# Performance work log

Measured on AMD Instinct MI355X. Metric: run time of the kernel, lower is better.

Reference implementation:

```python
import jax, jax.numpy as jnp
import numpy as np

NUM_OPS = 8
D = 1024
B = 8192


def setup_inputs() -> dict:
    key = jax.random.key(0)
    k1, k2, k3, k4 = jax.random.split(key, 4)
    x = jax.random.normal(k1, (B, D), dtype=jnp.float32)
    logits = 0.001 * jax.random.normal(k2, (NUM_OPS,), dtype=jnp.float32)
    Ws = jax.random.normal(k3, (NUM_OPS, D, D), dtype=jnp.float32) * (1.0 / np.sqrt(D))
    bs = jax.random.normal(k4, (NUM_OPS, D), dtype=jnp.float32) * 0.01
    return {"x": x, "logits": logits, "Ws": Ws, "bs": bs, "num_on_samples": 2}


def reference(x, logits, Ws, bs, num_on_samples):
    # non_stochastic_call: top-k op selection by architecture logits,
    # dispatch x to the selected ops, sum-combine the results.
    _, top_k_ids = jax.lax.top_k(logits, num_on_samples)  # [k]
    W_sel = jnp.take(Ws, top_k_ids, axis=0)  # [k, D, D]
    b_sel = jnp.take(bs, top_k_ids, axis=0)  # [k, D]
    # each op is Dense(D->D) + relu: [k, B, D]
    op_results = jax.nn.relu(jnp.einsum('bd,kde->kbe', x, W_sel) + b_sel[:, None, :])
    return jnp.sum(op_results, axis=0)  # [B, D]
```

## Files before the change

kernel.cpp:

```cpp
#include <hip/hip_runtime.h>
#include <hip/hip_bf16.h>

#define NUM_OPS 8
#define D 1024
#define B_ROWS 8192

typedef unsigned short ushort_t;
typedef __attribute__((ext_vector_type(8))) short bf16x8;
typedef __attribute__((ext_vector_type(4))) float f32x4;
typedef __attribute__((ext_vector_type(4))) float float4v;
typedef __attribute__((ext_vector_type(8))) unsigned short ushort8;

__device__ __forceinline__ unsigned short f2bf(float f) {
    union { float f; unsigned int u; } v; v.f = f;
    unsigned int u = v.u;
    unsigned int lsb = (u >> 16) & 1u;
    u += 0x7fffu + lsb;
    return (unsigned short)(u >> 16);
}

__device__ __forceinline__ void load_lds16(const void* g, void* l) {
    __builtin_amdgcn_global_load_lds(
        (const __attribute__((address_space(1))) void*)g,
        (__attribute__((address_space(3))) void*)l,
        16, 0, 0);
}

__device__ __forceinline__ void top2(const float* __restrict__ logits, int& i0, int& i1) {
    float best = -__builtin_inff(); i0 = 0;
    for (int i = 0; i < NUM_OPS; ++i) { float v = logits[i]; if (v > best) { best = v; i0 = i; } }
    float best2 = -__builtin_inff(); i1 = 0;
    for (int i = 0; i < NUM_OPS; ++i) {
        if (i == i0) continue;
        float v = logits[i]; if (v > best2) { best2 = v; i1 = i; }
    }
}

__global__ void prep_kernel(const float* __restrict__ x,
                            const float* __restrict__ Ws,
                            const float* __restrict__ logits,
                            ushort_t* __restrict__ xbf,
                            ushort_t* __restrict__ Wt) {
    __shared__ float t[32][33];
    const int bid = blockIdx.x;
    const int tid = threadIdx.x;
    if (bid < 4096) {
        int i = (bid * 256 + tid) * 8;
        float4v v0 = *(const float4v*)(x + i);
        float4v v1 = *(const float4v*)(x + i + 4);
        ushort8 o;
        o[0] = f2bf(v0[0]); o[1] = f2bf(v0[1]); o[2] = f2bf(v0[2]); o[3] = f2bf(v0[3]);
        o[4] = f2bf(v1[0]); o[5] = f2bf(v1[1]); o[6] = f2bf(v1[2]); o[7] = f2bf(v1[3]);
        *(ushort8*)(xbf + i) = o;
    } else {
        int i0, i1; top2(logits, i0, i1);
        const int b  = bid - 4096;
        const int e    = b >> 10;
        const int tile = b & 1023;
        const int td = (tile >> 5) << 5;
        const int te = (tile & 31) << 5;
        const int tx = tid & 31, ty = tid >> 5;
        const float* W = Ws + (size_t)(e ? i1 : i0) * D * D;
        for (int r = 0; r < 4; ++r)
            t[ty + 8 * r][tx] = W[(size_t)(td + ty + 8 * r) * D + te + tx];
        __syncthreads();
        ushort_t* o = Wt + (size_t)e * D * D;
        for (int r = 0; r < 4; ++r)
            o[(size_t)(te + ty + 8 * r) * D + td + tx] = f2bf(t[tx][ty + 8 * r]);
    }
}

__device__ __forceinline__ void stageA(const ushort_t* __restrict__ xbf, int brow,
                                       int u, ushort_t* dst, int tid) {
    #pragma unroll
    for (int q = 0; q < 4; ++q) {
        const int c   = q * 512 + tid;
        const int rr  = c >> 3;
        const int gcb = ((c & 7) * 16) ^ ((rr & 7) << 4);
        load_lds16(xbf + (size_t)(brow + rr) * D + u * 64 + (gcb >> 1), dst + c * 8);
    }
}
__device__ __forceinline__ void stageB(const ushort_t* __restrict__ Wt, int bcol,
                                       int u, ushort_t* dst, int tid) {
    #pragma unroll
    for (int q = 0; q < 2; ++q) {
        const int c   = q * 512 + tid;
        const int e   = c >> 9, cc = c & 511;
        const int n   = cc >> 3;
        const int gcb = ((cc & 7) * 16) ^ ((n & 7) << 4);
        load_lds16(Wt + (size_t)e * D * D + (size_t)(bcol + n) * D + u * 64 + (gcb >> 1),
                   dst + c * 8);
    }
}

#define SB()    __builtin_amdgcn_sched_barrier(0)
#define PRIO1() __builtin_amdgcn_s_setprio(1)
#define PRIO0() __builtin_amdgcn_s_setprio(0)
#define VMW(N)  do { asm volatile("s_waitcnt vmcnt(" #N ")" ::: "memory"); SB(); } while (0)
#define LGW(N)  do { asm volatile("s_waitcnt lgkmcnt(" #N ")" ::: "memory"); SB(); } while (0)
#define BAR()   do { __builtin_amdgcn_s_barrier(); SB(); } while (0)

#define DSR(dst, addr, imm)                                                    \
    asm volatile("ds_read_b128 %0, %1 offset:" #imm : "=v"(dst) : "v"(addr))

#define ISSUE_DS(P, SA, SBB)                                                   \
    do {                                                                       \
        unsigned aA0 = (unsigned)(size_t)(SA) + aro + x0;                      \
        unsigned aA1 = (unsigned)(size_t)(SA) + aro + x1;                      \
        unsigned aB0 = (unsigned)(size_t)(SBB) + bro + x0;                     \
        unsigned aB1 = (unsigned)(size_t)(SBB) + bro + x1;                     \
        DSR(P##a0, aA0, 0);    DSR(P##a1, aA0, 2048);                          \
        DSR(P##a2, aA0, 4096); DSR(P##a3, aA0, 6144);                          \
        DSR(P##a4, aA1, 0);    DSR(P##a5, aA1, 2048);                          \
        DSR(P##a6, aA1, 4096); DSR(P##a7, aA1, 6144);                          \
        DSR(P##b0, aB0, 0);    DSR(P##b1, aB0, 2048);                          \
        DSR(P##b4, aB0, 8192); DSR(P##b5, aB0, 10240);                         \
        DSR(P##b2, aB1, 0);    DSR(P##b3, aB1, 2048);                          \
        DSR(P##b6, aB1, 8192); DSR(P##b7, aB1, 10240);                         \
    } while (0)

#define MF(a, b, c) __builtin_amdgcn_mfma_f32_16x16x32_bf16(a, b, c, 0, 0, 0)
#define Q(P, A, B, E, M, N) acc[E][M][N] = MF(P##A, P##B, acc[E][M][N])

#define MFMA_SET(P)                                                            \
    do {                                                                       \
        PRIO1();                                                               \
        Q(P,a0,b0,0,0,0); Q(P,a0,b1,0,0,1); Q(P,a0,b4,1,0,0); Q(P,a0,b5,1,0,1);\
        Q(P,a1,b0,0,1,0); Q(P,a1,b1,0,1,1); Q(P,a1,b4,1,1,0); Q(P,a1,b5,1,1,1);\
        Q(P,a2,b0,0,2,0); Q(P,a2,b1,0,2,1); Q(P,a2,b4,1,2,0); Q(P,a2,b5,1,2,1);\
        Q(P,a3,b0,0,3,0); Q(P,a3,b1,0,3,1); Q(P,a3,b4,1,3,0); Q(P,a3,b5,1,3,1);\
        Q(P,a4,b2,0,0,0); Q(P,a4,b3,0,0,1); Q(P,a4,b6,1,0,0); Q(P,a4,b7,1,0,1);\
        Q(P,a5,b2,0,1,0); Q(P,a5,b3,0,1,1); Q(P,a5,b6,1,1,0); Q(P,a5,b7,1,1,1);\
        Q(P,a6,b2,0,2,0); Q(P,a6,b3,0,2,1); Q(P,a6,b6,1,2,0); Q(P,a6,b7,1,2,1);\
        Q(P,a7,b2,0,3,0); Q(P,a7,b3,0,3,1); Q(P,a7,b6,1,3,0); Q(P,a7,b7,1,3,1);\
        PRIO0();                                                               \
    } while (0)

#define TILE(SETN, SA, SBB, SU, DA, DB, SETC, DOSTG, VN)                       \
    do {                                                                       \
        VMW(VN);                                                               \
        BAR();                                                                 \
        ISSUE_DS(SETN, SA, SBB);                                               \
        SB();                                                                  \
        LGW(15);                                                               \
        if (DOSTG) { stageA(xbf, brow, (SU), DA, tid);                         \
                     stageB(Wt,  bcol, (SU), DB, tid); }                       \
        SB();                                                                  \
        MFMA_SET(SETC);                                                        \
        SB();                                                                  \
    } while (0)

__global__ __launch_bounds__(512, 2)
void gemm_dual(const ushort_t* __restrict__ xbf, const ushort_t* __restrict__ Wt,
               const float* __restrict__ bs, const float* __restrict__ logits,
               float* __restrict__ out) {
    __shared__ __align__(16) ushort_t As0[256 * 64], As1[256 * 64], As2[256 * 64];
    __shared__ __align__(16) ushort_t Bs0[2 * 64 * 64], Bs1[2 * 64 * 64], Bs2[2 * 64 * 64];

    const int tid  = threadIdx.x;
    const int wv   = tid >> 6;
    const int lane = tid & 63;
    const int rgrp = wv >> 1, cgrp = wv & 1;
    const int l15  = lane & 15, lq = lane >> 4;
    const int swz  = (l15 & 7) << 4;
    const int x0   = (lq * 16) ^ swz;
    const int x1   = (64 + lq * 16) ^ swz;
    const unsigned aro = (unsigned)((rgrp * 64 + l15) * 128);
    const unsigned bro = (unsigned)((cgrp * 32 + l15) * 128);

    const int bid  = blockIdx.x;
    const int brow = (bid & 31) * 256;
    const int bcol = (bid >> 5) * 64;

    f32x4 acc[2][4][2] = {};

    bf16x8 Xa0, Xa1, Xa2, Xa3, Xa4, Xa5, Xa6, Xa7;
    bf16x8 Xb0, Xb1, Xb2, Xb3, Xb4, Xb5, Xb6, Xb7;
    bf16x8 Ya0, Ya1, Ya2, Ya3, Ya4, Ya5, Ya6, Ya7;
    bf16x8 Yb0, Yb1, Yb2, Yb3, Yb4, Yb5, Yb6, Yb7;

    stageA(xbf, brow, 0, As0, tid); stageB(Wt, bcol, 0, Bs0, tid);
    stageA(xbf, brow, 1, As1, tid); stageB(Wt, bcol, 1, Bs1, tid);
    stageA(xbf, brow, 2, As2, tid); stageB(Wt, bcol, 2, Bs2, tid);
    SB();
    VMW(12);
    BAR();
    ISSUE_DS(X, As0, Bs0);
    SB();

    TILE(Y, As1, Bs1,  3, As0, Bs0, X, true,  6);
    TILE(X, As2, Bs2,  4, As1, Bs1, Y, true,  6);
    TILE(Y, As0, Bs0,  5, As2, Bs2, X, true,  6);
    TILE(X, As1, Bs1,  6, As0, Bs0, Y, true,  6);
    TILE(Y, As2, Bs2,  7, As1, Bs1, X, true,  6);
    TILE(X, As0, Bs0,  8, As2, Bs2, Y, true,  6);
    TILE(Y, As1, Bs1,  9, As0, Bs0, X, true,  6);
    TILE(X, As2, Bs2, 10, As1, Bs1, Y, true,  6);
    TILE(Y, As0, Bs0, 11, As2, Bs2, X, true,  6);
    TILE(X, As1, Bs1, 12, As0, Bs0, Y, true,  6);
    TILE(Y, As2, Bs2, 13, As1, Bs1, X, true,  6);
    TILE(X, As0, Bs0, 14, As2, Bs2, Y, true,  6);
    TILE(Y, As1, Bs1, 15, As0, Bs0, X, true,  6);
    TILE(X, As2, Bs2,  0, As0, Bs0, Y, false, 6);
    TILE(Y, As0, Bs0,  0, As0, Bs0, X, false, 0);
    LGW(0);
    MFMA_SET(Y);
    SB();

    int i0, i1; top2(logits, i0, i1);
    #pragma unroll
    for (int n16 = 0; n16 < 2; ++n16) {
        const int col = bcol + cgrp * 32 + n16 * 16 + l15;
        const float bb0 = bs[i0 * D + col];
        const float bb1 = bs[i1 * D + col];
        #pragma unroll
        for (int m = 0; m < 4; ++m) {
            const int rbase = brow + rgrp * 64 + m * 16 + lq * 4;
            #pragma unroll
            for (int i = 0; i < 4; ++i) {
                float v0 = acc[0][m][n16][i] + bb0; v0 = v0 > 0.f ? v0 : 0.f;
                float v1 = acc[1][m][n16][i] + bb1; v1 = v1 > 0.f ? v1 : 0.f;
                out[(size_t)(rbase + i) * D + col] = v0 + v1;
            }
        }
    }
}

extern "C" void kernel_launch(void* const* d_in, const int* in_sizes, int n_in,
                              void* d_out, int out_size, void* d_ws, size_t ws_size,
                              hipStream_t stream) {
    const float* x      = (const float*)d_in[0];
    const float* logits = (const float*)d_in[1];
    const float* Ws     = (const float*)d_in[2];
    const float* bs     = (const float*)d_in[3];
    float* out = (float*)d_out;

    char* ws = (char*)d_ws;
    ushort_t* xbf = (ushort_t*)ws;
    ushort_t* Wt  = (ushort_t*)(ws + (size_t)B_ROWS * D * 2);

    prep_kernel<<<4096 + 2048, 256, 0, stream>>>(x, Ws, logits, xbf, Wt);
    gemm_dual<<<512, 512, 0, stream>>>(xbf, Wt, bs, logits, out);
}
```

Before: 47.07 us.

## Pre-swizzle W into MFMA fragment layout and load B fragments directly to registers

The prep kernel now writes the selected weights in a per-lane MFMA fragment order instead of a plain transposed layout. The GEMM drops LDS staging for B and loads the B fragments straight from global memory into registers with dwordx4 loads issued after each MFMA set. This removes the LDS writes, reads and storage for B, but adds register pressure and exposes global load latency on the MFMA critical path, which the manual vmcnt wait counts must cover correctly.

```diff
diff --git a/kernel.cpp b/kernel.cpp
--- a/kernel.cpp
+++ b/kernel.cpp
@@ -40,7 +40,7 @@
                             const float* __restrict__ Ws,
                             const float* __restrict__ logits,
                             ushort_t* __restrict__ xbf,
-                            ushort_t* __restrict__ Wt) {
+                            ushort_t* __restrict__ Wf) {
     __shared__ float t[32][33];
     const int bid = blockIdx.x;
     const int tid = threadIdx.x;
@@ -53,20 +53,28 @@
         o[4] = f2bf(v1[0]); o[5] = f2bf(v1[1]); o[6] = f2bf(v1[2]); o[7] = f2bf(v1[3]);
         *(ushort8*)(xbf + i) = o;
     } else {
-        int i0, i1; top2(logits, i0, i1);
+        int s0, s1; top2(logits, s0, s1);
         const int b  = bid - 4096;
-        const int e    = b >> 10;
-        const int tile = b & 1023;
-        const int td = (tile >> 5) << 5;
-        const int te = (tile & 31) << 5;
+        const int nt = b & 31, kt = (b >> 5) & 31, e = b >> 10;
+        const int td = kt * 32, te = nt * 32;
         const int tx = tid & 31, ty = tid >> 5;
-        const float* W = Ws + (size_t)(e ? i1 : i0) * D * D;
+        const float* W = Ws + (size_t)(e ? s1 : s0) * D * D;
+        #pragma unroll
         for (int r = 0; r < 4; ++r)
             t[ty + 8 * r][tx] = W[(size_t)(td + ty + 8 * r) * D + te + tx];
         __syncthreads();
-        ushort_t* o = Wt + (size_t)e * D * D;
-        for (int r = 0; r < 4; ++r)
-            o[(size_t)(te + ty + 8 * r) * D + td + tx] = f2bf(t[tx][ty + 8 * r]);
+        if (tid < 128) {
+            const int n_l = tid & 31, kg = tid >> 5;
+            const int n = te + n_l, k0 = td + kg * 8;
+            const int u = k0 >> 6, kk = (k0 >> 5) & 1, lq = (k0 >> 3) & 3;
+            const int p = n >> 5, n16 = (n >> 4) & 1, l15 = n & 15;
+            const int lane = lq * 16 + l15;
+            const int fi = (((e * 32 + p) * 16 + u) * 2 + kk) * 2 + n16;
+            ushort8 o;
+            #pragma unroll
+            for (int j = 0; j < 8; ++j) o[j] = f2bf(t[kg * 8 + j][n_l]);
+            *(ushort8*)(Wf + (size_t)fi * 512 + lane * 8) = o;
+        }
     }
 }
 
@@ -80,18 +88,6 @@
         load_lds16(xbf + (size_t)(brow + rr) * D + u * 64 + (gcb >> 1), dst + c * 8);
     }
 }
-__device__ __forceinline__ void stageB(const ushort_t* __restrict__ Wt, int bcol,
-                                       int u, ushort_t* dst, int tid) {
-    #pragma unroll
-    for (int q = 0; q < 2; ++q) {
-        const int c   = q * 512 + tid;
-        const int e   = c >> 9, cc = c & 511;
-        const int n   = cc >> 3;
-        const int gcb = ((cc & 7) * 16) ^ ((n & 7) << 4);
-        load_lds16(Wt + (size_t)e * D * D + (size_t)(bcol + n) * D + u * 64 + (gcb >> 1),
-                   dst + c * 8);
-    }
-}
 
 #define SB()    __builtin_amdgcn_sched_barrier(0)
 #define PRIO1() __builtin_amdgcn_s_setprio(1)
@@ -102,21 +98,28 @@
 
 #define DSR(dst, addr, imm)                                                    \
     asm volatile("ds_read_b128 %0, %1 offset:" #imm : "=v"(dst) : "v"(addr))
-
-#define ISSUE_DS(P, SA, SBB)                                                   \
+#define GLD(dst, off, base, imm)                                               \
+    asm volatile("global_load_dwordx4 %0, %1, %2 offset:" #imm                 \
+                 : "=v"(dst) : "v"(off), "s"(base) : "memory")
+
+#define ISSUE_DSA(P, SA)                                                       \
     do {                                                                       \
         unsigned aA0 = (unsigned)(size_t)(SA) + aro + x0;                      \
         unsigned aA1 = (unsigned)(size_t)(SA) + aro + x1;                      \
-        unsigned aB0 = (unsigned)(size_t)(SBB) + bro + x0;                     \
-        unsigned aB1 = (unsigned)(size_t)(SBB) + bro + x1;                     \
         DSR(P##a0, aA0, 0);    DSR(P##a1, aA0, 2048);                          \
         DSR(P##a2, aA0, 4096); DSR(P##a3, aA0, 6144);                          \
         DSR(P##a4, aA1, 0);    DSR(P##a5, aA1, 2048);                          \
         DSR(P##a6, aA1, 4096); DSR(P##a7, aA1, 6144);                          \
-        DSR(P##b0, aB0, 0);    DSR(P##b1, aB0, 2048);                          \
-        DSR(P##b4, aB0, 8192); DSR(P##b5, aB0, 10240);                         \
-        DSR(P##b2, aB1, 0);    DSR(P##b3, aB1, 2048);                          \
-        DSR(P##b6, aB1, 8192); DSR(P##b7, aB1, 10240);                         \
+    } while (0)
+
+#define GLD_B(P, U)                                                            \
+    do {                                                                       \
+        unsigned vB  = boff + (unsigned)(U) * 4096u;                           \
+        unsigned vB2 = vB + 2097152u;                                          \
+        GLD(P##b0, vB,  Wf, 0);    GLD(P##b1, vB,  Wf, 1024);                  \
+        GLD(P##b2, vB,  Wf, 2048); GLD(P##b3, vB,  Wf, 3072);                  \
+        GLD(P##b4, vB2, Wf, 0);    GLD(P##b5, vB2, Wf, 1024);                  \
+        GLD(P##b6, vB2, Wf, 2048); GLD(P##b7, vB2, Wf, 3072);                  \
     } while (0)
 
 #define MF(a, b, c) __builtin_amdgcn_mfma_f32_16x16x32_bf16(a, b, c, 0, 0, 0)
@@ -136,26 +139,26 @@
         PRIO0();                                                               \
     } while (0)
 
-#define TILE(SETN, SA, SBB, SU, DA, DB, SETC, DOSTG, VN)                       \
+#define TILE(FN, FC, SRD, SU, DST, BU, DODS, DOSTG, DOGLD, VN)                 \
     do {                                                                       \
         VMW(VN);                                                               \
         BAR();                                                                 \
-        ISSUE_DS(SETN, SA, SBB);                                               \
-        SB();                                                                  \
-        LGW(15);                                                               \
-        if (DOSTG) { stageA(xbf, brow, (SU), DA, tid);                         \
-                     stageB(Wt,  bcol, (SU), DB, tid); }                       \
-        SB();                                                                  \
-        MFMA_SET(SETC);                                                        \
+        if (DODS) { ISSUE_DSA(FN, SRD); }                                      \
+        SB();                                                                  \
+        if (DODS) { LGW(8); } else { LGW(0); }                                 \
+        if (DOSTG) stageA(xbf, brow, (SU), DST, tid);                          \
+        SB();                                                                  \
+        MFMA_SET(FC);                                                          \
+        SB();                                                                  \
+        if (DOGLD) { GLD_B(FC, BU); }                                          \
         SB();                                                                  \
     } while (0)
 
 __global__ __launch_bounds__(512, 2)
-void gemm_dual(const ushort_t* __restrict__ xbf, const ushort_t* __restrict__ Wt,
+void gemm_dual(const ushort_t* __restrict__ xbf, const ushort_t* __restrict__ Wf,
                const float* __restrict__ bs, const float* __restrict__ logits,
                float* __restrict__ out) {
     __shared__ __align__(16) ushort_t As0[256 * 64], As1[256 * 64], As2[256 * 64];
-    __shared__ __align__(16) ushort_t Bs0[2 * 64 * 64], Bs1[2 * 64 * 64], Bs2[2 * 64 * 64];
 
     const int tid  = threadIdx.x;
     const int wv   = tid >> 6;
@@ -166,11 +169,12 @@
     const int x0   = (lq * 16) ^ swz;
     const int x1   = (64 + lq * 16) ^ swz;
     const unsigned aro = (unsigned)((rgrp * 64 + l15) * 128);
-    const unsigned bro = (unsigned)((cgrp * 32 + l15) * 128);
 
     const int bid  = blockIdx.x;
     const int brow = (bid & 31) * 256;
     const int bcol = (bid >> 5) * 64;
+    const int p    = (bid >> 5) * 2 + cgrp;
+    const unsigned boff = (unsigned)p * 65536u + (unsigned)lane * 16u;
 
     f32x4 acc[2][4][2] = {};
 
@@ -179,30 +183,33 @@
     bf16x8 Ya0, Ya1, Ya2, Ya3, Ya4, Ya5, Ya6, Ya7;
     bf16x8 Yb0, Yb1, Yb2, Yb3, Yb4, Yb5, Yb6, Yb7;
 
-    stageA(xbf, brow, 0, As0, tid); stageB(Wt, bcol, 0, Bs0, tid);
-    stageA(xbf, brow, 1, As1, tid); stageB(Wt, bcol, 1, Bs1, tid);
-    stageA(xbf, brow, 2, As2, tid); stageB(Wt, bcol, 2, Bs2, tid);
+    stageA(xbf, brow, 0, As0, tid);
+    GLD_B(X, 0); SB();
+    GLD_B(Y, 1); SB();
+    stageA(xbf, brow, 1, As1, tid);
+    stageA(xbf, brow, 2, As2, tid);
     SB();
-    VMW(12);
+    VMW(24);
     BAR();
-    ISSUE_DS(X, As0, Bs0);
+    ISSUE_DSA(X, As0);
     SB();
 
-    TILE(Y, As1, Bs1,  3, As0, Bs0, X, true,  6);
-    TILE(X, As2, Bs2,  4, As1, Bs1, Y, true,  6);
-    TILE(Y, As0, Bs0,  5, As2, Bs2, X, true,  6);
-    TILE(X, As1, Bs1,  6, As0, Bs0, Y, true,  6);
-    TILE(Y, As2, Bs2,  7, As1, Bs1, X, true,  6);
-    TILE(X, As0, Bs0,  8, As2, Bs2, Y, true,  6);
-    TILE(Y, As1, Bs1,  9, As0, Bs0, X, true,  6);
-    TILE(X, As2, Bs2, 10, As1, Bs1, Y, true,  6);
-    TILE(Y, As0, Bs0, 11, As2, Bs2, X, true,  6);
-    TILE(X, As1, Bs1, 12, As0, Bs0, Y, true,  6);
-    TILE(Y, As2, Bs2, 13, As1, Bs1, X, true,  6);
-    TILE(X, As0, Bs0, 14, As2, Bs2, Y, true,  6);
-    TILE(Y, As1, Bs1, 15, As0, Bs0, X, true,  6);
-    TILE(X, As2, Bs2,  0, As0, Bs0, Y, false, 6);
-    TILE(Y, As0, Bs0,  0, As0, Bs0, X, false, 0);
+    TILE(Y, X, As1,  3, As0,  2, 1, 1, 1,  4);
+    TILE(X, Y, As2,  4, As1,  3, 1, 1, 1, 12);
+    TILE(Y, X, As0,  5, As2,  4, 1, 1, 1, 12);
+    TILE(X, Y, As1,  6, As0,  5, 1, 1, 1, 12);
+    TILE(Y, X, As2,  7, As1,  6, 1, 1, 1, 12);
+    TILE(X, Y, As0,  8, As2,  7, 1, 1, 1, 12);
+    TILE(Y, X, As1,  9, As0,  8, 1, 1, 1, 12);
+    TILE(X, Y, As2, 10, As1,  9, 1, 1, 1, 12);
+    TILE(Y, X, As0, 11, As2, 10, 1, 1, 1, 12);
+    TILE(X, Y, As1, 12, As0, 11, 1, 1, 1, 12);
+    TILE(Y, X, As2, 13, As1, 12, 1, 1, 1, 12);
+    TILE(X, Y, As0, 14, As2, 13, 1, 1, 1, 12);
+    TILE(Y, X, As1, 15, As0, 14, 1, 1, 1, 12);
+    TILE(X, Y, As2,  0, As0, 15, 1, 0, 1, 12);
+    TILE(Y, X, As0,  0, As0,  0, 1, 0, 0,  8);
+    VMW(0);
     LGW(0);
     MFMA_SET(Y);
     SB();
@@ -237,8 +244,8 @@
 
     char* ws = (char*)d_ws;
     ushort_t* xbf = (ushort_t*)ws;
-    ushort_t* Wt  = (ushort_t*)(ws + (size_t)B_ROWS * D * 2);
-
-    prep_kernel<<<4096 + 2048, 256, 0, stream>>>(x, Ws, logits, xbf, Wt);
-    gemm_dual<<<512, 512, 0, stream>>>(xbf, Wt, bs, logits, out);
-}
+    ushort_t* Wf  = (ushort_t*)(ws + (size_t)B_ROWS * D * 2);
+
+    prep_kernel<<<4096 + 2048, 256, 0, stream>>>(x, Ws, logits, xbf, Wf);
+    gemm_dual<<<512, 512, 0, stream>>>(xbf, Wf, bs, logits, out);
+}
```

Measured after the change: 49.42 us. 1.05x slower.
